# Kernel tuning notes

Hardware: AMD Instinct MI355X
Metric: run time of the kernel (lower is better)

## Reference

```python
import jax, jax.numpy as jnp
import numpy as np

N, L, H = 64, 1024, 1024

def setup_inputs() -> dict:
    key = jax.random.key(0)
    ks = jax.random.split(key, 6)
    scale = 1.0 / np.sqrt(H)
    return {
        "decoder_hidden": jax.random.normal(ks[0], (N, H), dtype=jnp.float32),
        "encoder_hiddens": jax.random.normal(ks[1], (N, L, H), dtype=jnp.float32),
        "mask": jax.random.randint(ks[2], (N, L), 0, 2) > 0,  # True = PAD position
        "W_h": jax.random.normal(ks[3], (H, H), dtype=jnp.float32) * scale,
        "W_s": jax.random.normal(ks[4], (H, H), dtype=jnp.float32) * scale,
        "v": jax.random.normal(ks[5], (H,), dtype=jnp.float32) * scale,
    }

def reference(decoder_hidden, encoder_hiddens, mask, W_h, W_s, v):
    # score(h_t, h_s) = v^T tanh(W_h h_t + W_s h_s)
    # torch Linear: y = x @ W.T
    dh = decoder_hidden @ W_h.T                      # [N, H]
    eh = jnp.einsum('nlh,kh->nlk', encoder_hiddens, W_s)  # [N, L, H]
    score = jnp.tanh(dh[:, None, :] + eh) @ v        # [N, L]
    score = jnp.where(mask, -jnp.inf, score)
    attn_weights = jax.nn.softmax(score, axis=1)     # [N, L]
    context = jnp.einsum('nl,nlh->nh', attn_weights, encoder_hiddens)  # [N, H]
    return (context, attn_weights)
```

## Files before the change

### kernel.cpp

```cpp
#include <hip/hip_runtime.h>
#include <hip/hip_bf16.h>
#include <math.h>

#define N_  64
#define L_  1024
#define H_  1024
#define NL_ (N_ * L_)

typedef __attribute__((ext_vector_type(8))) short bf16x8;
typedef __attribute__((ext_vector_type(4))) float f32x4;
typedef unsigned short ushort_t;
typedef unsigned int uint_t;

__device__ inline ushort_t f32_to_bf16_rne(float f) {
    uint_t u = __float_as_uint(f);
    u += 0x7FFFu + ((u >> 16) & 1u);
    return (ushort_t)(u >> 16);
}

__global__ __launch_bounds__(256) void convert_bf16_kernel(const float* __restrict__ src,
                                                           ushort_t* __restrict__ dst,
                                                           size_t nvec8) {
    size_t stride = (size_t)gridDim.x * 256;
    for (size_t g = (size_t)blockIdx.x * 256 + threadIdx.x; g < nvec8; g += stride) {
        size_t i = g * 8;
        float4 a = *(const float4*)(src + i);
        float4 b = *(const float4*)(src + i + 4);
        union { bf16x8 v; ushort_t u[8]; } o;
        o.u[0] = f32_to_bf16_rne(a.x); o.u[1] = f32_to_bf16_rne(a.y);
        o.u[2] = f32_to_bf16_rne(a.z); o.u[3] = f32_to_bf16_rne(a.w);
        o.u[4] = f32_to_bf16_rne(b.x); o.u[5] = f32_to_bf16_rne(b.y);
        o.u[6] = f32_to_bf16_rne(b.z); o.u[7] = f32_to_bf16_rne(b.w);
        *(bf16x8*)(dst + i) = o.v;
    }
}

__global__ __launch_bounds__(256) void dh_kernel(const float* __restrict__ ddec,
                                                 const float* __restrict__ Wh,
                                                 float* __restrict__ dh) {
    int i = blockIdx.x * 256 + threadIdx.x;
    int n = i >> 10;
    const float* a = ddec + (size_t)n * H_;
    const float* w = Wh + (size_t)(i & (H_ - 1)) * H_;
    float acc = 0.f;
#pragma unroll 8
    for (int h = 0; h < H_; h += 4) {
        float4 av = *(const float4*)(a + h);
        float4 wv = *(const float4*)(w + h);
        acc += av.x * wv.x + av.y * wv.y + av.z * wv.z + av.w * wv.w;
    }
    dh[i] = acc;
}

__device__ inline void stage_tile(const ushort_t* __restrict__ gbase,
                                  ushort_t* lds, int tid, size_t row0_off) {
#pragma unroll
    for (int j = 0; j < 2; j++) {
        int c_lin = j * 256 + tid;
        int r  = c_lin >> 2;
        int cp = c_lin & 3;
        int q  = cp ^ ((r >> 1) & 3);
        const ushort_t* g = gbase + row0_off + (size_t)r * H_ + q * 8;
        ushort_t* l = lds + (size_t)(j * 256 + (tid & ~63)) * 8;
        __builtin_amdgcn_global_load_lds((const __attribute__((address_space(1))) void*)g,
                                         (__attribute__((address_space(3))) void*)l,
                                         16, 0, 0);
    }
}

__global__ __launch_bounds__(256) void score_mfma_kernel(const ushort_t* __restrict__ enc_bf,
                                                         const ushort_t* __restrict__ ws_bf,
                                                         const float* __restrict__ dh,
                                                         const float* __restrict__ v,
                                                         float* __restrict__ score) {
    __shared__ ushort_t As[128 * 32];
    __shared__ ushort_t Bs[128 * 32];

    const int b  = blockIdx.x;
    const int i0 = ((b & 7) | ((b >> 6) << 3)) * 128;
    const int k0 = ((b >> 3) & 7) * 128;
    const int tid  = threadIdx.x;
    const int lane = tid & 63;
    const int wv   = tid >> 6;
    const int wr   = (wv >> 1) * 64;
    const int wc   = (wv & 1) * 64;
    const int m    = lane & 15;
    const int q    = lane >> 4;
    const int qs   = q ^ ((m >> 1) & 3);

    f32x4 acc[4][4];
#pragma unroll
    for (int a = 0; a < 4; a++)
#pragma unroll
        for (int c = 0; c < 4; c++)
            acc[a][c] = (f32x4){0.f, 0.f, 0.f, 0.f};

    for (int h0 = 0; h0 < H_; h0 += 32) {
        __syncthreads();
        stage_tile(enc_bf, As, tid, (size_t)i0 * H_ + h0);
        stage_tile(ws_bf,  Bs, tid, (size_t)k0 * H_ + h0);
        __syncthreads();

        bf16x8 af[4], bfr[4];
#pragma unroll
        for (int ti = 0; ti < 4; ti++) {
            int r = wr + ti * 16 + m;
            af[ti] = *(const bf16x8*)(As + (size_t)(r * 4 + qs) * 8);
        }
#pragma unroll
        for (int tj = 0; tj < 4; tj++) {
            int r = wc + tj * 16 + m;
            bfr[tj] = *(const bf16x8*)(Bs + (size_t)(r * 4 + qs) * 8);
        }
#pragma unroll
        for (int ti = 0; ti < 4; ti++)
#pragma unroll
            for (int tj = 0; tj < 4; tj++)
                acc[ti][tj] = __builtin_amdgcn_mfma_f32_16x16x32_bf16(
                    af[ti], bfr[tj], acc[ti][tj], 0, 0, 0);
    }

    const int nb = i0 >> 10;
    float vv[4], dhv[4];
#pragma unroll
    for (int tj = 0; tj < 4; tj++) {
        int k = k0 + wc + tj * 16 + m;
        vv[tj]  = v[k];
        dhv[tj] = dh[nb * H_ + k];
    }
#pragma unroll
    for (int ti = 0; ti < 4; ti++) {
#pragma unroll
        for (int reg = 0; reg < 4; reg++) {
            float s = 0.f;
#pragma unroll
            for (int tj = 0; tj < 4; tj++) {
                float x  = dhv[tj] + acc[ti][tj][reg];
                float e2 = __expf(2.f * x);
                s += vv[tj] * (1.f - 2.f / (e2 + 1.f));
            }
            s += __shfl_xor(s, 1);
            s += __shfl_xor(s, 2);
            s += __shfl_xor(s, 4);
            s += __shfl_xor(s, 8);
            if (m == 0) {
                int i_local = wr + ti * 16 + q * 4 + reg;
                atomicAdd(&score[i0 + i_local], s);
            }
        }
    }
}

__global__ __launch_bounds__(256) void softmax_kernel(const float* __restrict__ score,
                                                      const int* __restrict__ mask,
                                                      float* __restrict__ attn) {
    const int n = blockIdx.x;
    const int t = threadIdx.x;
    __shared__ float redmax[4];
    __shared__ float redsum[4];

    float s[4];
    int   mk[4];
    float mymax = -INFINITY;
#pragma unroll
    for (int j = 0; j < 4; j++) {
        int l = t + j * 256;
        mk[j] = mask[n * L_ + l];
        s[j] = mk[j] ? -INFINITY : score[n * L_ + l];
        mymax = fmaxf(mymax, s[j]);
    }
#pragma unroll
    for (int off = 1; off < 64; off <<= 1)
        mymax = fmaxf(mymax, __shfl_xor(mymax, off));
    if ((t & 63) == 0) redmax[t >> 6] = mymax;
    __syncthreads();
    float gmax = fmaxf(fmaxf(redmax[0], redmax[1]), fmaxf(redmax[2], redmax[3]));

    float e[4];
    float mysum = 0.f;
#pragma unroll
    for (int j = 0; j < 4; j++) {
        e[j] = mk[j] ? 0.f : __expf(s[j] - gmax);
        mysum += e[j];
    }
#pragma unroll
    for (int off = 1; off < 64; off <<= 1)
        mysum += __shfl_xor(mysum, off);
    if ((t & 63) == 0) redsum[t >> 6] = mysum;
    __syncthreads();
    float gsum = redsum[0] + redsum[1] + redsum[2] + redsum[3];
    float inv = 1.f / gsum;
#pragma unroll
    for (int j = 0; j < 4; j++)
        attn[n * L_ + t + j * 256] = e[j] * inv;
}

__global__ __launch_bounds__(128) void context_kernel(const ushort_t* __restrict__ enc_bf,
                                                      const float* __restrict__ attn,
                                                      float* __restrict__ ctx) {
    const int n  = blockIdx.x;
    const int l0 = blockIdx.y * 128;
    const int t  = threadIdx.x;
    const int h0 = t * 8;

    __shared__ float w[128];
    w[t] = attn[n * L_ + l0 + t];
    __syncthreads();

    const ushort_t* base = enc_bf + (size_t)n * L_ * H_ + (size_t)l0 * H_ + h0;
    float acc[8] = {};
#pragma unroll 4
    for (int l = 0; l < 128; l++) {
        union { bf16x8 v; ushort_t u[8]; } e;
        e.v = *(const bf16x8*)(base + (size_t)l * H_);
        float wl = w[l];
#pragma unroll
        for (int j = 0; j < 8; j++)
            acc[j] += wl * __uint_as_float(((uint_t)e.u[j]) << 16);
    }
#pragma unroll
    for (int j = 0; j < 8; j++)
        atomicAdd(&ctx[n * H_ + h0 + j], acc[j]);
}

extern "C" void kernel_launch(void* const* d_in, const int* in_sizes, int n_in,
                              void* d_out, int out_size, void* d_ws, size_t ws_size,
                              hipStream_t stream) {
    const float* ddec = (const float*)d_in[0];
    const float* enc  = (const float*)d_in[1];
    const int*   mask = (const int*)d_in[2];
    const float* Wh   = (const float*)d_in[3];
    const float* Ws   = (const float*)d_in[4];
    const float* v    = (const float*)d_in[5];

    float* out_ctx  = (float*)d_out;
    float* out_attn = out_ctx + N_ * H_;

    ushort_t* enc_bf = (ushort_t*)d_ws;
    ushort_t* ws_bf  = enc_bf + (size_t)NL_ * H_;
    float*    dh     = (float*)(ws_bf + (size_t)H_ * H_);
    float*    score  = dh + N_ * H_;

    convert_bf16_kernel<<<4096, 256, 0, stream>>>(enc, enc_bf, (size_t)NL_ * H_ / 8);
    convert_bf16_kernel<<<512, 256, 0, stream>>>(Ws, ws_bf, (size_t)H_ * H_ / 8);

    hipMemsetAsync(score, 0, (size_t)NL_ * sizeof(float), stream);
    hipMemsetAsync(out_ctx, 0, (size_t)N_ * H_ * sizeof(float), stream);

    dh_kernel<<<NL_ / 256, 256, 0, stream>>>(ddec, Wh, dh);

    score_mfma_kernel<<<4096, 256, 0, stream>>>(enc_bf, ws_bf, dh, v, score);

    softmax_kernel<<<N_, 256, 0, stream>>>(score, mask, out_attn);

    dim3 g4(N_, 8);
    context_kernel<<<g4, 128, 0, stream>>>(enc_bf, out_attn, out_ctx);
}
```

Before: 659.7 us.

## Fuse encoder bf16 conversion into score GEMM tile staging and read fp32 in context

Drops the standalone pass that converted the full encoder tensor to bf16. The score GEMM now loads fp32 encoder tiles directly, truncates them to bf16 in registers and writes them to LDS. The context kernel reads fp32 encoder values, using 256 threads with four columns each. This removes a full read plus a bf16 write of the large encoder tensor, but each encoder tile is now re-read as fp32 by all 8 column blocks in the GEMM, which doubles the bytes per load and replaces the async global-to-LDS copies with register staging. It also switches from round-to-nearest to truncation.

Result: slower. 675.1 us (+2.3%).

```diff
diff --git a/kernel.cpp b/kernel.cpp
--- a/kernel.cpp
+++ b/kernel.cpp
@@ -52,8 +52,12 @@
     dh[i] = acc;
 }
 
-__device__ inline void stage_tile(const ushort_t* __restrict__ gbase,
-                                  ushort_t* lds, int tid, size_t row0_off) {
+__device__ inline uint_t pack_bf16_trunc(float lo, float hi) {
+    return __builtin_amdgcn_perm(__float_as_uint(hi), __float_as_uint(lo), 0x07060302u);
+}
+
+__device__ inline void stage_tile_bf16(const ushort_t* __restrict__ gbase,
+                                       ushort_t* lds, int tid, size_t row0_off) {
 #pragma unroll
     for (int j = 0; j < 2; j++) {
         int c_lin = j * 256 + tid;
@@ -68,7 +72,7 @@
     }
 }
 
-__global__ __launch_bounds__(256) void score_mfma_kernel(const ushort_t* __restrict__ enc_bf,
+__global__ __launch_bounds__(256) void score_mfma_kernel(const float* __restrict__ enc,
                                                          const ushort_t* __restrict__ ws_bf,
                                                          const float* __restrict__ dh,
                                                          const float* __restrict__ v,
@@ -97,8 +101,23 @@
 
     for (int h0 = 0; h0 < H_; h0 += 32) {
         __syncthreads();
-        stage_tile(enc_bf, As, tid, (size_t)i0 * H_ + h0);
-        stage_tile(ws_bf,  Bs, tid, (size_t)k0 * H_ + h0);
+        stage_tile_bf16(ws_bf, Bs, tid, (size_t)k0 * H_ + h0);
+#pragma unroll
+        for (int j = 0; j < 2; j++) {
+            int c_lin = j * 256 + tid;
+            int r  = c_lin >> 2;
+            int cp = c_lin & 3;
+            int qg = cp ^ ((r >> 1) & 3);
+            const float* g = enc + (size_t)(i0 + r) * H_ + h0 + qg * 8;
+            float4 fa = *(const float4*)g;
+            float4 fb = *(const float4*)(g + 4);
+            uint4 o;
+            o.x = pack_bf16_trunc(fa.x, fa.y);
+            o.y = pack_bf16_trunc(fa.z, fa.w);
+            o.z = pack_bf16_trunc(fb.x, fb.y);
+            o.w = pack_bf16_trunc(fb.z, fb.w);
+            *(uint4*)(As + (size_t)c_lin * 8) = o;
+        }
         __syncthreads();
 
         bf16x8 af[4], bfr[4];
@@ -195,32 +214,30 @@
         attn[n * L_ + t + j * 256] = e[j] * inv;
 }
 
-__global__ __launch_bounds__(128) void context_kernel(const ushort_t* __restrict__ enc_bf,
+__global__ __launch_bounds__(256) void context_kernel(const float* __restrict__ enc,
                                                       const float* __restrict__ attn,
                                                       float* __restrict__ ctx) {
     const int n  = blockIdx.x;
     const int l0 = blockIdx.y * 128;
     const int t  = threadIdx.x;
-    const int h0 = t * 8;
+    const int h0 = t * 4;
 
     __shared__ float w[128];
-    w[t] = attn[n * L_ + l0 + t];
+    if (t < 128) w[t] = attn[n * L_ + l0 + t];
     __syncthreads();
 
-    const ushort_t* base = enc_bf + (size_t)n * L_ * H_ + (size_t)l0 * H_ + h0;
-    float acc[8] = {};
-#pragma unroll 4
+    const float* base = enc + ((size_t)n * L_ + l0) * H_ + h0;
+    float ax = 0.f, ay = 0.f, az = 0.f, aw = 0.f;
+#pragma unroll 8
     for (int l = 0; l < 128; l++) {
-        union { bf16x8 v; ushort_t u[8]; } e;
-        e.v = *(const bf16x8*)(base + (size_t)l * H_);
+        float4 e = *(const float4*)(base + (size_t)l * H_);
         float wl = w[l];
-#pragma unroll
-        for (int j = 0; j < 8; j++)
-            acc[j] += wl * __uint_as_float(((uint_t)e.u[j]) << 16);
-    }
-#pragma unroll
-    for (int j = 0; j < 8; j++)
-        atomicAdd(&ctx[n * H_ + h0 + j], acc[j]);
+        ax += wl * e.x; ay += wl * e.y; az += wl * e.z; aw += wl * e.w;
+    }
+    atomicAdd(&ctx[n * H_ + h0 + 0], ax);
+    atomicAdd(&ctx[n * H_ + h0 + 1], ay);
+    atomicAdd(&ctx[n * H_ + h0 + 2], az);
+    atomicAdd(&ctx[n * H_ + h0 + 3], aw);
 }
 
 extern "C" void kernel_launch(void* const* d_in, const int* in_sizes, int n_in,
@@ -236,12 +253,10 @@
     float* out_ctx  = (float*)d_out;
     float* out_attn = out_ctx + N_ * H_;
 
-    ushort_t* enc_bf = (ushort_t*)d_ws;
-    ushort_t* ws_bf  = enc_bf + (size_t)NL_ * H_;
-    float*    dh     = (float*)(ws_bf + (size_t)H_ * H_);
-    float*    score  = dh + N_ * H_;
-
-    convert_bf16_kernel<<<4096, 256, 0, stream>>>(enc, enc_bf, (size_t)NL_ * H_ / 8);
+    ushort_t* ws_bf = (ushort_t*)d_ws;
+    float*    dh    = (float*)(ws_bf + (size_t)H_ * H_);
+    float*    score = dh + N_ * H_;
+
     convert_bf16_kernel<<<512, 256, 0, stream>>>(Ws, ws_bf, (size_t)H_ * H_ / 8);
 
     hipMemsetAsync(score, 0, (size_t)NL_ * sizeof(float), stream);
@@ -249,10 +264,10 @@
 
     dh_kernel<<<NL_ / 256, 256, 0, stream>>>(ddec, Wh, dh);
 
-    score_mfma_kernel<<<4096, 256, 0, stream>>>(enc_bf, ws_bf, dh, v, score);
+    score_mfma_kernel<<<4096, 256, 0, stream>>>(enc, ws_bf, dh, v, score);
 
     softmax_kernel<<<N_, 256, 0, stream>>>(score, mask, out_attn);
 
     dim3 g4(N_, 8);
-    context_kernel<<<g4, 128, 0, stream>>>(enc_bf, out_attn, out_ctx);
-}
+    context_kernel<<<g4, 256, 0, stream>>>(enc, out_attn, out_ctx);
+}
```
